# Kernel optimization log

Hardware: AMD Instinct MI355X
Metric: run time of the kernel (lower is better)

## Reference

```python
import jax, jax.numpy as jnp
import numpy as np

D = 128  # embed dim

def linear(x, W, b):
    return x @ W.T + b

def mha1(x, w_in, b_in, w_out, b_out):
    # Single-head MultiheadAttention, x: (S, B, D), seq-first like torch.nn.MultiheadAttention
    q, k, v = jnp.split(x @ w_in.T + b_in, 3, axis=-1)
    scores = jnp.einsum('sbd,tbd->bst', q, k) / jnp.sqrt(jnp.asarray(D, x.dtype))
    att = jax.nn.softmax(scores, axis=-1)
    o = jnp.einsum('bst,tbd->sbd', att, v)
    return o @ w_out.T + b_out

def setup_inputs() -> dict:
    key = jax.random.key(0)
    ks = iter(jax.random.split(key, 32))
    def p(shape, scale=0.02):
        return (jax.random.normal(next(ks), shape, dtype=jnp.float32) * scale)
    B, S, F = 8, 2048, 3584
    inp = {
        'x': jax.random.normal(next(ks), (B, S, F), dtype=jnp.float32),
        'place_W': p((128, 2048)), 'place_b': p((128,)),
        'cast_W': p((128, 512)), 'cast_b': p((128,)),
        'action_W': p((128, 512)), 'action_b': p((128,)),
        'audio_W': p((128, 512)), 'audio_b': p((128,)),
        'e_W': p((128, 512)), 'e_b': p((128,)),
        'la_win': p((3 * D, D)), 'la_bin': p((3 * D,)),
        'la_wout': p((D, D)), 'la_bout': p((D,)),
        'be_W': p((128, 256)), 'be_b': p((128,)),
        'ba_win': p((3 * D, D)), 'ba_bin': p((3 * D,)),
        'ba_wout': p((D, D)), 'ba_bout': p((D,)),
        'bp_W': p((1, 128)), 'bp_b': p((1,)),
    }
    return inp

def reference(x, place_W, place_b, cast_W, cast_b, action_W, action_b,
              audio_W, audio_b, e_W, e_b, la_win, la_bin, la_wout, la_bout,
              be_W, be_b, ba_win, ba_bin, ba_wout, ba_bout, bp_W, bp_b):
    # --- forward_embeddings ---
    place = jax.nn.relu(linear(x[:, :, :2048], place_W, place_b))
    cast = jax.nn.relu(linear(x[:, :, 2048:2560], cast_W, cast_b))
    action = jax.nn.relu(linear(x[:, :, 2560:3072], action_W, action_b))
    audio = jax.nn.relu(linear(x[:, :, 3072:3584], audio_W, audio_b))
    feats = jnp.concatenate((place, cast, action, audio), axis=2)  # (B,S,512)
    e = jax.nn.relu(linear(feats, e_W, e_b))  # (B,S,128)
    e = jnp.transpose(e, (1, 0, 2))  # (S,B,128) seq-first
    e = mha1(e, la_win, la_bin, la_wout, la_bout)
    # --- forward_segmentation (single-pass prefix/suffix means) ---
    S = e.shape[0]
    csum = jnp.cumsum(e, axis=0)  # (S,B,D)
    total = csum[-1]
    i = jnp.arange(1, S, dtype=e.dtype)[:, None, None]
    left = csum[:-1] / i                       # mean of e[:i]
    right = (total[None] - csum[:-1]) / (S - i)  # mean of e[i:]
    cat = jnp.concatenate((left, right), axis=-1)  # (S-1,B,256)
    b = jax.nn.relu(linear(cat, be_W, be_b))
    b = mha1(b, ba_win, ba_bin, ba_wout, ba_bout)
    b = jax.nn.sigmoid(linear(b, bp_W, bp_b))[..., 0]  # (S-1,B)
    return (e, b)
```

## Files before the change

kernel.cpp:

```cpp
#include <hip/hip_runtime.h>
#include <hip/hip_bf16.h>
#include <math.h>
#include <stdint.h>


#define DEV static __device__ __forceinline__

typedef __attribute__((ext_vector_type(8))) short bf16x8;
typedef __attribute__((ext_vector_type(4))) float f32x4;

DEV uint32_t pk2bf(float a, float b) {
  __hip_bfloat162 h = __float22bfloat162_rn(make_float2(a, b));
  return *(uint32_t*)&h;
}
DEV uint2 cvt4(float4 f) {
  return make_uint2(pk2bf(f.x, f.y), pk2bf(f.z, f.w));
}
DEV uint16_t bf1(float a) { return (uint16_t)(pk2bf(a, 0.f) & 0xffffu); }
DEV float frombf(uint16_t h) {
  union { uint32_t u; float f; } v; v.u = ((uint32_t)h) << 16; return v.f;
}

#define OFF_PW      0u
#define OFF_CW      262144u
#define OFF_AW      327680u
#define OFF_UW      393216u
#define OFF_EW      458752u
#define OFF_LAWIN   524288u
#define OFF_LAWOUT  573440u
#define OFF_BEW     589824u
#define OFF_BAWIN   622592u
#define OFF_BAWOUT  671744u
#define OFF_END     688128u

struct WPtrs { const float* p[10]; };

__global__ __launch_bounds__(256) void pack_weights(WPtrs wp, uint16_t* __restrict__ WB)
{
  const uint32_t off[11] = {OFF_PW, OFF_CW, OFF_AW, OFF_UW, OFF_EW, OFF_LAWIN,
                            OFF_LAWOUT, OFF_BEW, OFF_BAWIN, OFF_BAWOUT, OFF_END};
  uint32_t h = (blockIdx.x * 256u + threadIdx.x) * 4u;
  if (h >= OFF_END) return;
  int s = 0;
  while (h >= off[s + 1]) ++s;
  float4 f = *(const float4*)(wp.p[s] + (h - off[s]));
  *(uint2*)(WB + h) = cvt4(f);
}

template<bool ABF, bool OBF, bool RELU, bool REMAP>
__global__ __launch_bounds__(256) void gemm64(
    const void* __restrict__ Ap, int lda,
    const uint16_t* __restrict__ Wb,
    const float* __restrict__ bias,
    void* __restrict__ Cp, int ldc,
    int M, int K)
{
  __shared__ __align__(16) uint16_t As[64 * 72];
  __shared__ __align__(16) uint16_t Ws[128 * 72];

  const int t  = threadIdx.x;
  const int m0 = blockIdx.x * 64;
  const int n0 = blockIdx.y * 128;
  const int w  = t >> 6, l = t & 63;
  const int ln = l & 15, qd = l >> 4;

  f32x4 acc[4][2];
#pragma unroll
  for (int i = 0; i < 4; ++i) { acc[i][0] = (f32x4){0,0,0,0}; acc[i][1] = (f32x4){0,0,0,0}; }

  const int rr = t >> 4;
  const int cl = (t & 15) * 4;
  const int r8 = t >> 3;
  const int c8 = (t & 7) * 8;

  for (int k0 = 0; k0 < K; k0 += 64) {
    __syncthreads();
    if (ABF) {
      const uint16_t* A = (const uint16_t*)Ap;
#pragma unroll
      for (int i = 0; i < 2; ++i) {
        int m = m0 + r8 + 32 * i;
        int mc = m < M ? m : M - 1;
        *(bf16x8*)(As + (size_t)(r8 + 32 * i) * 72 + c8) =
            *(const bf16x8*)(A + (size_t)mc * lda + k0 + c8);
      }
    } else {
      const float* A = (const float*)Ap;
#pragma unroll
      for (int i = 0; i < 4; ++i) {
        int m = m0 + rr + 16 * i;
        int mc = m < M ? m : M - 1;
        float4 f = *(const float4*)(A + (size_t)mc * lda + k0 + cl);
        *(uint2*)(As + (size_t)(rr + 16 * i) * 72 + cl) = cvt4(f);
      }
    }
#pragma unroll
    for (int i = 0; i < 4; ++i) {
      int n = r8 + 32 * i;
      *(bf16x8*)(Ws + (size_t)n * 72 + c8) =
          *(const bf16x8*)(Wb + (size_t)(n0 + n) * K + k0 + c8);
    }
    __syncthreads();
#pragma unroll
    for (int ks = 0; ks < 2; ++ks) {
      bf16x8 af[4], bfr[2];
#pragma unroll
      for (int mf = 0; mf < 4; ++mf)
        af[mf] = *(const bf16x8*)(As + (size_t)(mf * 16 + ln) * 72 + ks * 32 + qd * 8);
#pragma unroll
      for (int nf = 0; nf < 2; ++nf)
        bfr[nf] = *(const bf16x8*)(Ws + (size_t)(w * 32 + nf * 16 + ln) * 72 + ks * 32 + qd * 8);
#pragma unroll
      for (int mf = 0; mf < 4; ++mf)
#pragma unroll
        for (int nf = 0; nf < 2; ++nf)
          acc[mf][nf] = __builtin_amdgcn_mfma_f32_16x16x32_bf16(af[mf], bfr[nf], acc[mf][nf], 0, 0, 0);
    }
  }

#pragma unroll
  for (int mf = 0; mf < 4; ++mf) {
#pragma unroll
    for (int r = 0; r < 4; ++r) {
      int m = m0 + mf * 16 + qd * 4 + r;
      if (m < M) {
        size_t ro = REMAP ? (size_t)((m & 2047) * 8 + (m >> 11)) : (size_t)m;
#pragma unroll
        for (int nf = 0; nf < 2; ++nf) {
          int n = n0 + w * 32 + nf * 16 + ln;
          float v = acc[mf][nf][r] + bias[n];
          if (RELU) v = fmaxf(v, 0.f);
          if (OBF) ((uint16_t*)Cp)[ro * (size_t)ldc + n] = bf1(v);
          else     ((float*)Cp)[ro * (size_t)ldc + n] = v;
        }
      }
    }
  }
}

__global__ __launch_bounds__(256) void gemm_feats64(
    const float* __restrict__ x, const uint16_t* __restrict__ WB,
    const float* __restrict__ pb, const float* __restrict__ cb,
    const float* __restrict__ ab, const float* __restrict__ ub,
    uint16_t* __restrict__ feats)
{
  __shared__ __align__(16) uint16_t As[64 * 72];
  __shared__ __align__(16) uint16_t Ws[128 * 72];

  const int seg = blockIdx.y;
  const uint16_t* Wb; const float* bias; int kbase, Kseg;
  if (seg == 0)      { Wb = WB + OFF_PW; bias = pb; kbase = 0;    Kseg = 2048; }
  else if (seg == 1) { Wb = WB + OFF_CW; bias = cb; kbase = 2048; Kseg = 512; }
  else if (seg == 2) { Wb = WB + OFF_AW; bias = ab; kbase = 2560; Kseg = 512; }
  else               { Wb = WB + OFF_UW; bias = ub; kbase = 3072; Kseg = 512; }

  const int t  = threadIdx.x;
  const int m0 = blockIdx.x * 64;
  const int w  = t >> 6, l = t & 63;
  const int ln = l & 15, qd = l >> 4;

  f32x4 acc[4][2];
#pragma unroll
  for (int i = 0; i < 4; ++i) { acc[i][0] = (f32x4){0,0,0,0}; acc[i][1] = (f32x4){0,0,0,0}; }

  const int rr = t >> 4;
  const int cl = (t & 15) * 4;
  const int r8 = t >> 3;
  const int c8 = (t & 7) * 8;

  for (int k0 = 0; k0 < Kseg; k0 += 64) {
    __syncthreads();
#pragma unroll
    for (int i = 0; i < 4; ++i) {
      int m = m0 + rr + 16 * i;
      float4 f = *(const float4*)(x + (size_t)m * 3584 + kbase + k0 + cl);
      *(uint2*)(As + (size_t)(rr + 16 * i) * 72 + cl) = cvt4(f);
    }
#pragma unroll
    for (int i = 0; i < 4; ++i) {
      int n = r8 + 32 * i;
      *(bf16x8*)(Ws + (size_t)n * 72 + c8) =
          *(const bf16x8*)(Wb + (size_t)n * Kseg + k0 + c8);
    }
    __syncthreads();
#pragma unroll
    for (int ks = 0; ks < 2; ++ks) {
      bf16x8 af[4], bfr[2];
#pragma unroll
      for (int mf = 0; mf < 4; ++mf)
        af[mf] = *(const bf16x8*)(As + (size_t)(mf * 16 + ln) * 72 + ks * 32 + qd * 8);
#pragma unroll
      for (int nf = 0; nf < 2; ++nf)
        bfr[nf] = *(const bf16x8*)(Ws + (size_t)(w * 32 + nf * 16 + ln) * 72 + ks * 32 + qd * 8);
#pragma unroll
      for (int mf = 0; mf < 4; ++mf)
#pragma unroll
        for (int nf = 0; nf < 2; ++nf)
          acc[mf][nf] = __builtin_amdgcn_mfma_f32_16x16x32_bf16(af[mf], bfr[nf], acc[mf][nf], 0, 0, 0);
    }
  }

#pragma unroll
  for (int mf = 0; mf < 4; ++mf) {
#pragma unroll
    for (int r = 0; r < 4; ++r) {
      int m = m0 + mf * 16 + qd * 4 + r;
#pragma unroll
      for (int nf = 0; nf < 2; ++nf) {
        int n = w * 32 + nf * 16 + ln;
        float v = fmaxf(acc[mf][nf][r] + bias[n], 0.f);
        feats[(size_t)m * 512 + seg * 128 + n] = bf1(v);
      }
    }
  }
}

__global__ __launch_bounds__(256) void gemm_becat64(
    const float* __restrict__ csum,
    const uint16_t* __restrict__ Wb, const float* __restrict__ bias,
    uint16_t* __restrict__ C)
{
  __shared__ __align__(16) uint16_t As[64 * 72];
  __shared__ __align__(16) uint16_t Ws[128 * 72];

  const int M = 16376, K = 256;
  const int t  = threadIdx.x;
  const int m0 = blockIdx.x * 64;
  const int w  = t >> 6, l = t & 63;
  const int ln = l & 15, qd = l >> 4;

  f32x4 acc[4][2];
#pragma unroll
  for (int i = 0; i < 4; ++i) { acc[i][0] = (f32x4){0,0,0,0}; acc[i][1] = (f32x4){0,0,0,0}; }

  const int rr = t >> 4;
  const int cl = (t & 15) * 4;
  const int r8 = t >> 3;
  const int c8 = (t & 7) * 8;

  for (int k0 = 0; k0 < K; k0 += 64) {
    __syncthreads();
#pragma unroll
    for (int i = 0; i < 4; ++i) {
      int m = m0 + rr + 16 * i;
      int mc = m < M ? m : M - 1;
      int j = mc >> 3, bb = mc & 7;
      int kk = k0 + cl;
      float4 f;
      if (kk < 128) {
        float4 v = *(const float4*)(csum + (size_t)mc * 128 + kk);
        float s = 1.f / (float)(j + 1);
        f = make_float4(v.x * s, v.y * s, v.z * s, v.w * s);
      } else {
        int d = kk - 128;
        float4 c0 = *(const float4*)(csum + (size_t)mc * 128 + d);
        float4 ct = *(const float4*)(csum + (size_t)(16376 + bb) * 128 + d);
        float s = 1.f / (float)(2047 - j);
        f = make_float4((ct.x - c0.x) * s, (ct.y - c0.y) * s,
                        (ct.z - c0.z) * s, (ct.w - c0.w) * s);
      }
      *(uint2*)(As + (size_t)(rr + 16 * i) * 72 + cl) = cvt4(f);
    }
#pragma unroll
    for (int i = 0; i < 4; ++i) {
      int n = r8 + 32 * i;
      *(bf16x8*)(Ws + (size_t)n * 72 + c8) =
          *(const bf16x8*)(Wb + (size_t)n * K + k0 + c8);
    }
    __syncthreads();
#pragma unroll
    for (int ks = 0; ks < 2; ++ks) {
      bf16x8 af[4], bfr[2];
#pragma unroll
      for (int mf = 0; mf < 4; ++mf)
        af[mf] = *(const bf16x8*)(As + (size_t)(mf * 16 + ln) * 72 + ks * 32 + qd * 8);
#pragma unroll
      for (int nf = 0; nf < 2; ++nf)
        bfr[nf] = *(const bf16x8*)(Ws + (size_t)(w * 32 + nf * 16 + ln) * 72 + ks * 32 + qd * 8);
#pragma unroll
      for (int mf = 0; mf < 4; ++mf)
#pragma unroll
        for (int nf = 0; nf < 2; ++nf)
          acc[mf][nf] = __builtin_amdgcn_mfma_f32_16x16x32_bf16(af[mf], bfr[nf], acc[mf][nf], 0, 0, 0);
    }
  }

#pragma unroll
  for (int mf = 0; mf < 4; ++mf) {
#pragma unroll
    for (int r = 0; r < 4; ++r) {
      int m = m0 + mf * 16 + qd * 4 + r;
      if (m < M) {
#pragma unroll
        for (int nf = 0; nf < 2; ++nf) {
          int n = w * 32 + nf * 16 + ln;
          C[(size_t)m * 128 + n] = bf1(fmaxf(acc[mf][nf][r] + bias[n], 0.f));
        }
      }
    }
  }
}

__global__ __launch_bounds__(256) void vpack(
    const uint16_t* __restrict__ proj, uint16_t* __restrict__ Vtb, int Slen)
{
  __shared__ __align__(16) uint16_t Vs[64][136];

  const int kt = blockIdx.x, b = blockIdx.y, t = threadIdx.x;
  const int sl = t >> 2, cg = (t & 3) * 32;
  const int s  = kt * 64 + sl;
  const int valid = s < Slen;
  const int sc = valid ? s : Slen - 1;
  const uint16_t* src = proj + ((size_t)sc * 8 + b) * 384 + 256 + cg;
#pragma unroll
  for (int i = 0; i < 4; ++i) {
    bf16x8 v;
    if (valid) v = *(const bf16x8*)(src + i * 8);
    else       v = (bf16x8){0,0,0,0,0,0,0,0};
    *(bf16x8*)(&Vs[sl][cg + i * 8]) = v;
  }
  __syncthreads();
  const int d = t >> 1, hh = t & 1;
  uint32_t wv[16];
#pragma unroll
  for (int j = 0; j < 8; ++j) {
    int k0o = hh * 8 + j;
    wv[j * 2]     = (uint32_t)Vs[k0o][d]      | ((uint32_t)Vs[k0o + 16][d] << 16);
    wv[j * 2 + 1] = (uint32_t)Vs[k0o + 32][d] | ((uint32_t)Vs[k0o + 48][d] << 16);
  }
  uint16_t* dv = Vtb + (((size_t)b * 32 + kt) * 128 + d) * 64 + hh * 32;
#pragma unroll
  for (int i = 0; i < 4; ++i)
    *(uint4*)(dv + i * 8) = *(uint4*)(&wv[i * 4]);
}

__global__ __launch_bounds__(256, 3) void attn_split3(
    const uint16_t* __restrict__ proj, const uint16_t* __restrict__ Vtb,
    float* __restrict__ Opart, float* __restrict__ ml, int Slen)
{
  __shared__ __align__(16) uint16_t KsL[64 * 136];
  __shared__ __align__(16) uint16_t VtL[128 * 72];
  __shared__ __align__(16) uint16_t PbL[4][16 * 72];

  const int t  = threadIdx.x;
  const int b  = blockIdx.y;
  const int q0 = blockIdx.x * 64;
  const int split = blockIdx.z;
  const int kbeg = split * 704;
  const int kend = (split == 2) ? Slen : kbeg + 704;
  const int w  = t >> 6;
  const int l  = t & 63;
  const int ln = l & 15;
  const int qd = l >> 4;
  const float scl = 0.08838834764831845f;

  bf16x8 qf[4];
  {
    int qrow = q0 + w * 16 + ln;
    int qc = qrow < Slen ? qrow : Slen - 1;
    const uint16_t* qp = proj + ((size_t)qc * 8 + b) * 384 + qd * 8;
#pragma unroll
    for (int ks = 0; ks < 4; ++ks) {
      union { bf16x8 v; uint16_t h[8]; uint32_t u[4]; } in, out;
      in.v = *(const bf16x8*)(qp + ks * 32);
#pragma unroll
      for (int j = 0; j < 4; ++j)
        out.u[j] = pk2bf(frombf(in.h[2 * j]) * scl, frombf(in.h[2 * j + 1]) * scl);
      qf[ks] = out.v;
    }
  }

  f32x4 oacc[8];
#pragma unroll
  for (int i = 0; i < 8; ++i) oacc[i] = (f32x4){0.f, 0.f, 0.f, 0.f};
  float mrow[4] = {-INFINITY, -INFINITY, -INFINITY, -INFINITY};
  float lrow[4] = {0.f, 0.f, 0.f, 0.f};

  const int ntiles = (kend - kbeg + 63) >> 6;
  for (int kt = 0; kt < ntiles; ++kt) {
    __syncthreads();
    {
      const int key = t >> 2, cg = (t & 3) * 32;
      int kg = kbeg + kt * 64 + key;
      int kc = kg < Slen ? kg : Slen - 1;
      const uint16_t* src = proj + ((size_t)kc * 8 + b) * 384 + 128 + cg;
      uint16_t* dst = KsL + key * 136 + cg;
#pragma unroll
      for (int i = 0; i < 4; ++i)
        *(bf16x8*)(dst + i * 8) = *(const bf16x8*)(src + i * 8);
    }
    {
      const int d = t >> 1, h2 = (t & 1) * 32;
      const int tile = 11 * split + kt;
      const uint16_t* src = Vtb + (((size_t)b * 32 + tile) * 128 + d) * 64 + h2;
      uint16_t* dst = VtL + d * 72 + h2;
#pragma unroll
      for (int i = 0; i < 4; ++i)
        *(bf16x8*)(dst + i * 8) = *(const bf16x8*)(src + i * 8);
    }
    __syncthreads();

    f32x4 sc[4];
#pragma unroll
    for (int nf = 0; nf < 4; ++nf) {
      f32x4 acc = (f32x4){0.f, 0.f, 0.f, 0.f};
#pragma unroll
      for (int ks = 0; ks < 4; ++ks) {
        bf16x8 kf = *(const bf16x8*)(KsL + (size_t)(nf * 16 + ln) * 136 + ks * 32 + qd * 8);
        acc = __builtin_amdgcn_mfma_f32_16x16x32_bf16(qf[ks], kf, acc, 0, 0, 0);
      }
      int key = kbeg + kt * 64 + nf * 16 + ln;
      if (key >= kend) { acc[0] = -1e30f; acc[1] = -1e30f; acc[2] = -1e30f; acc[3] = -1e30f; }
      sc[nf] = acc;
    }

    float alphaR[4];
#pragma unroll
    for (int r = 0; r < 4; ++r) {
      float mx = fmaxf(fmaxf(sc[0][r], sc[1][r]), fmaxf(sc[2][r], sc[3][r]));
      mx = fmaxf(mx, __shfl_xor(mx, 1));
      mx = fmaxf(mx, __shfl_xor(mx, 2));
      mx = fmaxf(mx, __shfl_xor(mx, 4));
      mx = fmaxf(mx, __shfl_xor(mx, 8));
      float mNew = fmaxf(mrow[r], mx);
      float p0 = __expf(sc[0][r] - mNew);
      float p1 = __expf(sc[1][r] - mNew);
      float p2 = __expf(sc[2][r] - mNew);
      float p3 = __expf(sc[3][r] - mNew);
      float ps = p0 + p1 + p2 + p3;
      ps += __shfl_xor(ps, 1);
      ps += __shfl_xor(ps, 2);
      ps += __shfl_xor(ps, 4);
      ps += __shfl_xor(ps, 8);
      float alpha = __expf(mrow[r] - mNew);
      mrow[r] = mNew;
      lrow[r] = lrow[r] * alpha + ps;
      alphaR[r] = alpha;
      uint2 pk;
      pk.x = pk2bf(p0, p1);
      pk.y = pk2bf(p2, p3);
      *(uint2*)(PbL[w] + (size_t)(qd * 4 + r) * 72 + ln * 4) = pk;
    }
#pragma unroll
    for (int no = 0; no < 8; ++no) {
#pragma unroll
      for (int r = 0; r < 4; ++r) oacc[no][r] *= alphaR[r];
    }
    __asm__ volatile("s_waitcnt lgkmcnt(0)" ::: "memory");

#pragma unroll
    for (int ks2 = 0; ks2 < 2; ++ks2) {
      bf16x8 af = *(const bf16x8*)(PbL[w] + (size_t)ln * 72 + ks2 * 32 + qd * 8);
#pragma unroll
      for (int no = 0; no < 8; ++no) {
        bf16x8 vf = *(const bf16x8*)(VtL + (size_t)(no * 16 + ln) * 72 + ks2 * 32 + qd * 8);
        oacc[no] = __builtin_amdgcn_mfma_f32_16x16x32_bf16(af, vf, oacc[no], 0, 0, 0);
      }
    }
  }

#pragma unroll
  for (int r = 0; r < 4; ++r) {
    int qg = q0 + w * 16 + qd * 4 + r;
    if (qg < Slen) {
      size_t row = (size_t)qg * 8 + b;
      float* dst = Opart + ((size_t)split * 16384 + row) * 128 + ln;
#pragma unroll
      for (int no = 0; no < 8; ++no) dst[no * 16] = oacc[no][r];
      if (ln == 0) {
        ml[((size_t)split * 16384 + row) * 2 + 0] = mrow[r];
        ml[((size_t)split * 16384 + row) * 2 + 1] = lrow[r];
      }
    }
  }
}

__global__ __launch_bounds__(256) void attn_combine3(
    const float* __restrict__ Opart, const float* __restrict__ ml,
    uint16_t* __restrict__ out, int rows)
{
  int idx = blockIdx.x * 256 + threadIdx.x;
  int row = idx >> 5;
  int d   = (idx & 31) * 4;
  if (row >= rows) return;
  float m0 = ml[(size_t)row * 2],                 l0 = ml[(size_t)row * 2 + 1];
  float m1 = ml[((size_t)16384 + row) * 2],       l1 = ml[((size_t)16384 + row) * 2 + 1];
  float m2 = ml[((size_t)32768 + row) * 2],       l2 = ml[((size_t)32768 + row) * 2 + 1];
  float M = fmaxf(fmaxf(m0, m1), m2);
  float w0 = __expf(m0 - M), w1 = __expf(m1 - M), w2 = __expf(m2 - M);
  float inv = 1.f / (l0 * w0 + l1 * w1 + l2 * w2);
  float4 a = *(const float4*)(Opart + (size_t)row * 128 + d);
  float4 c = *(const float4*)(Opart + ((size_t)16384 + row) * 128 + d);
  float4 e = *(const float4*)(Opart + ((size_t)32768 + row) * 128 + d);
  float4 o = make_float4((a.x * w0 + c.x * w1 + e.x * w2) * inv,
                         (a.y * w0 + c.y * w1 + e.y * w2) * inv,
                         (a.z * w0 + c.z * w1 + e.z * w2) * inv,
                         (a.w * w0 + c.w * w1 + e.w * w2) * inv);
  *(uint2*)(out + (size_t)row * 128 + d) = cvt4(o);
}

__global__ void cumsum_p1(const float* __restrict__ e, float* __restrict__ csum,
                          float* __restrict__ part)
{
  int chunk = blockIdx.x, b = blockIdx.y, d = threadIdx.x;
  float run = 0.f;
  int s0 = chunk * 64;
  for (int s = 0; s < 64; ++s) {
    size_t idx = ((size_t)(s0 + s) * 8 + b) * 128 + d;
    run += e[idx];
    csum[idx] = run;
  }
  part[(b * 32 + chunk) * 128 + d] = run;
}

__global__ void cumsum_p2(float* __restrict__ part)
{
  int b = blockIdx.x, d = threadIdx.x;
  float run = 0.f;
  for (int c = 0; c < 32; ++c) {
    float v = part[(b * 32 + c) * 128 + d];
    part[(b * 32 + c) * 128 + d] = run;
    run += v;
  }
}

__global__ void cumsum_p3(float* __restrict__ csum, const float* __restrict__ part)
{
  int chunk = blockIdx.x, b = blockIdx.y, d = threadIdx.x;
  float off = part[(b * 32 + chunk) * 128 + d];
  int s0 = chunk * 64;
  for (int s = 0; s < 64; ++s)
    csum[((size_t)(s0 + s) * 8 + b) * 128 + d] += off;
}

__global__ __launch_bounds__(256) void gemm_bout_head(
    const uint16_t* __restrict__ A,
    const uint16_t* __restrict__ Wb,
    const float* __restrict__ bias,
    const float* __restrict__ bpW, const float* __restrict__ bpb,
    float* __restrict__ out, int M)
{
  __shared__ __align__(16) uint16_t As[64 * 72];
  __shared__ __align__(16) uint16_t Ws[128 * 72];
  __shared__ float Ct[64][133];

  const int K = 128;
  const int t  = threadIdx.x;
  const int m0 = blockIdx.x * 64;
  const int w  = t >> 6, l = t & 63;
  const int ln = l & 15, qd = l >> 4;

  f32x4 acc[4][2];
#pragma unroll
  for (int i = 0; i < 4; ++i) { acc[i][0] = (f32x4){0,0,0,0}; acc[i][1] = (f32x4){0,0,0,0}; }

  const int r8 = t >> 3;
  const int c8 = (t & 7) * 8;

  for (int k0 = 0; k0 < K; k0 += 64) {
    __syncthreads();
#pragma unroll
    for (int i = 0; i < 2; ++i) {
      int m = m0 + r8 + 32 * i;
      int mc = m < M ? m : M - 1;
      *(bf16x8*)(As + (size_t)(r8 + 32 * i) * 72 + c8) =
          *(const bf16x8*)(A + (size_t)mc * 128 + k0 + c8);
    }
#pragma unroll
    for (int i = 0; i < 4; ++i) {
      int n = r8 + 32 * i;
      *(bf16x8*)(Ws + (size_t)n * 72 + c8) =
          *(const bf16x8*)(Wb + (size_t)n * K + k0 + c8);
    }
    __syncthreads();
#pragma unroll
    for (int ks = 0; ks < 2; ++ks) {
      bf16x8 af[4], bfr[2];
#pragma unroll
      for (int mf = 0; mf < 4; ++mf)
        af[mf] = *(const bf16x8*)(As + (size_t)(mf * 16 + ln) * 72 + ks * 32 + qd * 8);
#pragma unroll
      for (int nf = 0; nf < 2; ++nf)
        bfr[nf] = *(const bf16x8*)(Ws + (size_t)(w * 32 + nf * 16 + ln) * 72 + ks * 32 + qd * 8);
#pragma unroll
      for (int mf = 0; mf < 4; ++mf)
#pragma unroll
        for (int nf = 0; nf < 2; ++nf)
          acc[mf][nf] = __builtin_amdgcn_mfma_f32_16x16x32_bf16(af[mf], bfr[nf], acc[mf][nf], 0, 0, 0);
    }
  }

  __syncthreads();
#pragma unroll
  for (int mf = 0; mf < 4; ++mf) {
#pragma unroll
    for (int r = 0; r < 4; ++r) {
      int rowL = mf * 16 + qd * 4 + r;
#pragma unroll
      for (int nf = 0; nf < 2; ++nf) {
        int n = w * 32 + nf * 16 + ln;
        Ct[rowL][n] = acc[mf][nf][r] + bias[n];
      }
    }
  }
  __syncthreads();
  {
    int row = t >> 2, qg = t & 3;
    int m = m0 + row;
    float p = 0.f;
#pragma unroll
    for (int j = 0; j < 32; ++j) {
      int c = qg + j * 4;
      p += Ct[row][c] * bpW[c];
    }
    p += __shfl_xor(p, 1);
    p += __shfl_xor(p, 2);
    if (qg == 0 && m < M)
      out[m] = 1.f / (1.f + __expf(-(p + bpb[0])));
  }
}

extern "C" void kernel_launch(void* const* d_in, const int* in_sizes, int n_in,
                              void* d_out, int out_size, void* d_ws, size_t ws_size,
                              hipStream_t stream)
{
  const float* x       = (const float*)d_in[0];
  const float* pW      = (const float*)d_in[1];
  const float* pb      = (const float*)d_in[2];
  const float* cW      = (const float*)d_in[3];
  const float* cb      = (const float*)d_in[4];
  const float* aW      = (const float*)d_in[5];
  const float* ab      = (const float*)d_in[6];
  const float* uW      = (const float*)d_in[7];
  const float* ub      = (const float*)d_in[8];
  const float* eW      = (const float*)d_in[9];
  const float* eb      = (const float*)d_in[10];
  const float* la_win  = (const float*)d_in[11];
  const float* la_bin  = (const float*)d_in[12];
  const float* la_wout = (const float*)d_in[13];
  const float* la_bout = (const float*)d_in[14];
  const float* beW     = (const float*)d_in[15];
  const float* beb     = (const float*)d_in[16];
  const float* ba_win  = (const float*)d_in[17];
  const float* ba_bin  = (const float*)d_in[18];
  const float* ba_wout = (const float*)d_in[19];
  const float* ba_bout = (const float*)d_in[20];
  const float* bpW     = (const float*)d_in[21];
  const float* bpb     = (const float*)d_in[22];

  float* ws   = (float*)d_ws;
  float* outF = (float*)d_out;

  uint16_t* WB  = (uint16_t*)ws;
  float* base   = ws + 344064;
  uint16_t* featsB = (uint16_t*)base;
  float* csumB  = base;
  float* partB  = base + 2097152;
  uint16_t* eB  = (uint16_t*)(base + 4194304);
  uint16_t* projB = (uint16_t*)(base + 5242880);
  uint16_t* VtbB  = (uint16_t*)(base + 8388608);
  float* OpartB = base + 9437184;
  float* mlB    = base + 15728640;

  WPtrs wp;
  wp.p[0] = pW; wp.p[1] = cW; wp.p[2] = aW; wp.p[3] = uW; wp.p[4] = eW;
  wp.p[5] = la_win; wp.p[6] = la_wout; wp.p[7] = beW; wp.p[8] = ba_win; wp.p[9] = ba_wout;
  pack_weights<<<dim3(672), 256, 0, stream>>>(wp, WB);

  gemm_feats64<<<dim3(256, 4), 256, 0, stream>>>(x, WB, pb, cb, ab, ub, featsB);
  gemm64<true, true, true, true><<<dim3(256, 1), 256, 0, stream>>>(
      featsB, 512, WB + OFF_EW, eb, eB, 128, 16384, 512);
  gemm64<true, true, false, false><<<dim3(256, 3), 256, 0, stream>>>(
      eB, 128, WB + OFF_LAWIN, la_bin, projB, 384, 16384, 128);
  vpack<<<dim3(32, 8), 256, 0, stream>>>(projB, VtbB, 2048);
  attn_split3<<<dim3(32, 8, 3), 256, 0, stream>>>(projB, VtbB, OpartB, mlB, 2048);
  attn_combine3<<<dim3(2048), 256, 0, stream>>>(OpartB, mlB, eB, 16384);
  gemm64<true, false, false, false><<<dim3(256, 1), 256, 0, stream>>>(
      eB, 128, WB + OFF_LAWOUT, la_bout, outF, 128, 16384, 128);
  cumsum_p1<<<dim3(32, 8), 128, 0, stream>>>(outF, csumB, partB);
  cumsum_p2<<<dim3(8), 128, 0, stream>>>(partB);
  cumsum_p3<<<dim3(32, 8), 128, 0, stream>>>(csumB, partB);
  gemm_becat64<<<dim3(256), 256, 0, stream>>>(csumB, WB + OFF_BEW, beb, eB);
  gemm64<true, true, false, false><<<dim3(256, 3), 256, 0, stream>>>(
      eB, 128, WB + OFF_BAWIN, ba_bin, projB, 384, 16376, 128);
  vpack<<<dim3(32, 8), 256, 0, stream>>>(projB, VtbB, 2047);
  attn_split3<<<dim3(32, 8, 3), 256, 0, stream>>>(projB, VtbB, OpartB, mlB, 2047);
  attn_combine3<<<dim3(2047), 256, 0, stream>>>(OpartB, mlB, eB, 16376);
  gemm_bout_head<<<dim3(256), 256, 0, stream>>>(
      eB, WB + OFF_BAWOUT, ba_bout, bpW, bpb, outF + 2097152, 16376);
}
```

Measured before the change: 553.4 us.

## Fuse attention combine into out-proj GEMM, fold cumsum fixup, prefetch K/V

The split-attention combine step now happens inside the output-projection GEMM's A-tile load, which drops the separate combine kernel and its bf16 round trip for both attention blocks. The third cumsum pass is removed: the boundary GEMM adds the per-chunk prefix offsets itself, and the cumsum now uses 32-row chunks to launch more blocks. The attention kernel also register-prefetches the next K/V tile while the current one is computed. In exchange the GEMM does extra reads of three Opart slices and the partial array, and the prefetch raises register pressure.

Result: faster. 537.2 us (-2.9%).

```diff
diff --git a/kernel.cpp b/kernel.cpp
--- a/kernel.cpp
+++ b/kernel.cpp
@@ -216,7 +216,7 @@
 }
 
 __global__ __launch_bounds__(256) void gemm_becat64(
-    const float* __restrict__ csum,
+    const float* __restrict__ csum, const float* __restrict__ part,
     const uint16_t* __restrict__ Wb, const float* __restrict__ bias,
     uint16_t* __restrict__ C)
 {
@@ -249,15 +249,21 @@
       float4 f;
       if (kk < 128) {
         float4 v = *(const float4*)(csum + (size_t)mc * 128 + kk);
+        float4 p = *(const float4*)(part + (size_t)(bb * 64 + (j >> 5)) * 128 + kk);
         float s = 1.f / (float)(j + 1);
-        f = make_float4(v.x * s, v.y * s, v.z * s, v.w * s);
+        f = make_float4((v.x + p.x) * s, (v.y + p.y) * s,
+                        (v.z + p.z) * s, (v.w + p.w) * s);
       } else {
         int d = kk - 128;
         float4 c0 = *(const float4*)(csum + (size_t)mc * 128 + d);
+        float4 p0 = *(const float4*)(part + (size_t)(bb * 64 + (j >> 5)) * 128 + d);
         float4 ct = *(const float4*)(csum + (size_t)(16376 + bb) * 128 + d);
+        float4 pt = *(const float4*)(part + (size_t)(bb * 64 + 63) * 128 + d);
         float s = 1.f / (float)(2047 - j);
-        f = make_float4((ct.x - c0.x) * s, (ct.y - c0.y) * s,
-                        (ct.z - c0.z) * s, (ct.w - c0.w) * s);
+        f = make_float4(((ct.x + pt.x) - (c0.x + p0.x)) * s,
+                        ((ct.y + pt.y) - (c0.y + p0.y)) * s,
+                        ((ct.z + pt.z) - (c0.z + p0.z)) * s,
+                        ((ct.w + pt.w) - (c0.w + p0.w)) * s);
       }
       *(uint2*)(As + (size_t)(rr + 16 * i) * 72 + cl) = cvt4(f);
     }
@@ -354,6 +360,9 @@
   const int qd = l >> 4;
   const float scl = 0.08838834764831845f;
 
+  const int kkey = t >> 2, kcg = (t & 3) * 32;
+  const int vd   = t >> 1, vh  = (t & 1) * 32;
+
   bf16x8 qf[4];
   {
     int qrow = q0 + w * 16 + ln;
@@ -377,26 +386,39 @@
   float lrow[4] = {0.f, 0.f, 0.f, 0.f};
 
   const int ntiles = (kend - kbeg + 63) >> 6;
+
+  bf16x8 kreg[4], vreg[4];
+  {
+    int kg = kbeg + kkey;
+    int kc = kg < Slen ? kg : Slen - 1;
+    const uint16_t* ksrc = proj + ((size_t)kc * 8 + b) * 384 + 128 + kcg;
+#pragma unroll
+    for (int i = 0; i < 4; ++i) kreg[i] = *(const bf16x8*)(ksrc + i * 8);
+    const uint16_t* vsrc = Vtb + (((size_t)b * 32 + 11 * split) * 128 + vd) * 64 + vh;
+#pragma unroll
+    for (int i = 0; i < 4; ++i) vreg[i] = *(const bf16x8*)(vsrc + i * 8);
+  }
+
   for (int kt = 0; kt < ntiles; ++kt) {
     __syncthreads();
     {
-      const int key = t >> 2, cg = (t & 3) * 32;
-      int kg = kbeg + kt * 64 + key;
+      uint16_t* kdst = KsL + kkey * 136 + kcg;
+#pragma unroll
+      for (int i = 0; i < 4; ++i) *(bf16x8*)(kdst + i * 8) = kreg[i];
+      uint16_t* vdst = VtL + vd * 72 + vh;
+#pragma unroll
+      for (int i = 0; i < 4; ++i) *(bf16x8*)(vdst + i * 8) = vreg[i];
+    }
+    if (kt + 1 < ntiles) {
+      int kg = kbeg + (kt + 1) * 64 + kkey;
       int kc = kg < Slen ? kg : Slen - 1;
-      const uint16_t* src = proj + ((size_t)kc * 8 + b) * 384 + 128 + cg;
-      uint16_t* dst = KsL + key * 136 + cg;
-#pragma unroll
-      for (int i = 0; i < 4; ++i)
-        *(bf16x8*)(dst + i * 8) = *(const bf16x8*)(src + i * 8);
-    }
-    {
-      const int d = t >> 1, h2 = (t & 1) * 32;
-      const int tile = 11 * split + kt;
-      const uint16_t* src = Vtb + (((size_t)b * 32 + tile) * 128 + d) * 64 + h2;
-      uint16_t* dst = VtL + d * 72 + h2;
-#pragma unroll
-      for (int i = 0; i < 4; ++i)
-        *(bf16x8*)(dst + i * 8) = *(const bf16x8*)(src + i * 8);
+      const uint16_t* ksrc = proj + ((size_t)kc * 8 + b) * 384 + 128 + kcg;
+#pragma unroll
+      for (int i = 0; i < 4; ++i) kreg[i] = *(const bf16x8*)(ksrc + i * 8);
+      const int tile = 11 * split + kt + 1;
+      const uint16_t* vsrc = Vtb + (((size_t)b * 32 + tile) * 128 + vd) * 64 + vh;
+#pragma unroll
+      for (int i = 0; i < 4; ++i) vreg[i] = *(const bf16x8*)(vsrc + i * 8);
     }
     __syncthreads();
 
@@ -475,66 +497,9 @@
   }
 }
 
-__global__ __launch_bounds__(256) void attn_combine3(
+template<bool HEAD>
+__global__ __launch_bounds__(256) void gemm_attc64(
     const float* __restrict__ Opart, const float* __restrict__ ml,
-    uint16_t* __restrict__ out, int rows)
-{
-  int idx = blockIdx.x * 256 + threadIdx.x;
-  int row = idx >> 5;
-  int d   = (idx & 31) * 4;
-  if (row >= rows) return;
-  float m0 = ml[(size_t)row * 2],                 l0 = ml[(size_t)row * 2 + 1];
-  float m1 = ml[((size_t)16384 + row) * 2],       l1 = ml[((size_t)16384 + row) * 2 + 1];
-  float m2 = ml[((size_t)32768 + row) * 2],       l2 = ml[((size_t)32768 + row) * 2 + 1];
-  float M = fmaxf(fmaxf(m0, m1), m2);
-  float w0 = __expf(m0 - M), w1 = __expf(m1 - M), w2 = __expf(m2 - M);
-  float inv = 1.f / (l0 * w0 + l1 * w1 + l2 * w2);
-  float4 a = *(const float4*)(Opart + (size_t)row * 128 + d);
-  float4 c = *(const float4*)(Opart + ((size_t)16384 + row) * 128 + d);
-  float4 e = *(const float4*)(Opart + ((size_t)32768 + row) * 128 + d);
-  float4 o = make_float4((a.x * w0 + c.x * w1 + e.x * w2) * inv,
-                         (a.y * w0 + c.y * w1 + e.y * w2) * inv,
-                         (a.z * w0 + c.z * w1 + e.z * w2) * inv,
-                         (a.w * w0 + c.w * w1 + e.w * w2) * inv);
-  *(uint2*)(out + (size_t)row * 128 + d) = cvt4(o);
-}
-
-__global__ void cumsum_p1(const float* __restrict__ e, float* __restrict__ csum,
-                          float* __restrict__ part)
-{
-  int chunk = blockIdx.x, b = blockIdx.y, d = threadIdx.x;
-  float run = 0.f;
-  int s0 = chunk * 64;
-  for (int s = 0; s < 64; ++s) {
-    size_t idx = ((size_t)(s0 + s) * 8 + b) * 128 + d;
-    run += e[idx];
-    csum[idx] = run;
-  }
-  part[(b * 32 + chunk) * 128 + d] = run;
-}
-
-__global__ void cumsum_p2(float* __restrict__ part)
-{
-  int b = blockIdx.x, d = threadIdx.x;
-  float run = 0.f;
-  for (int c = 0; c < 32; ++c) {
-    float v = part[(b * 32 + c) * 128 + d];
-    part[(b * 32 + c) * 128 + d] = run;
-    run += v;
-  }
-}
-
-__global__ void cumsum_p3(float* __restrict__ csum, const float* __restrict__ part)
-{
-  int chunk = blockIdx.x, b = blockIdx.y, d = threadIdx.x;
-  float off = part[(b * 32 + chunk) * 128 + d];
-  int s0 = chunk * 64;
-  for (int s = 0; s < 64; ++s)
-    csum[((size_t)(s0 + s) * 8 + b) * 128 + d] += off;
-}
-
-__global__ __launch_bounds__(256) void gemm_bout_head(
-    const uint16_t* __restrict__ A,
     const uint16_t* __restrict__ Wb,
     const float* __restrict__ bias,
     const float* __restrict__ bpW, const float* __restrict__ bpb,
@@ -542,7 +507,8 @@
 {
   __shared__ __align__(16) uint16_t As[64 * 72];
   __shared__ __align__(16) uint16_t Ws[128 * 72];
-  __shared__ float Ct[64][133];
+  __shared__ float RW[64][4];
+  __shared__ float Ct[HEAD ? 64 : 1][133];
 
   const int K = 128;
   const int t  = threadIdx.x;
@@ -550,21 +516,44 @@
   const int w  = t >> 6, l = t & 63;
   const int ln = l & 15, qd = l >> 4;
 
+  if (t < 64) {
+    int m = m0 + t;
+    int mc = m < M ? m : M - 1;
+    float m0v = ml[(size_t)mc * 2],                 l0 = ml[(size_t)mc * 2 + 1];
+    float m1v = ml[((size_t)16384 + mc) * 2],       l1 = ml[((size_t)16384 + mc) * 2 + 1];
+    float m2v = ml[((size_t)32768 + mc) * 2],       l2 = ml[((size_t)32768 + mc) * 2 + 1];
+    float Mx = fmaxf(fmaxf(m0v, m1v), m2v);
+    float w0 = __expf(m0v - Mx), w1 = __expf(m1v - Mx), w2 = __expf(m2v - Mx);
+    RW[t][0] = w0; RW[t][1] = w1; RW[t][2] = w2;
+    RW[t][3] = 1.f / (l0 * w0 + l1 * w1 + l2 * w2);
+  }
+
   f32x4 acc[4][2];
 #pragma unroll
   for (int i = 0; i < 4; ++i) { acc[i][0] = (f32x4){0,0,0,0}; acc[i][1] = (f32x4){0,0,0,0}; }
 
+  const int rr = t >> 4;
+  const int cl = (t & 15) * 4;
   const int r8 = t >> 3;
   const int c8 = (t & 7) * 8;
 
   for (int k0 = 0; k0 < K; k0 += 64) {
     __syncthreads();
 #pragma unroll
-    for (int i = 0; i < 2; ++i) {
-      int m = m0 + r8 + 32 * i;
+    for (int i = 0; i < 4; ++i) {
+      int m = m0 + rr + 16 * i;
       int mc = m < M ? m : M - 1;
-      *(bf16x8*)(As + (size_t)(r8 + 32 * i) * 72 + c8) =
-          *(const bf16x8*)(A + (size_t)mc * 128 + k0 + c8);
+      int kk = k0 + cl;
+      float4 a = *(const float4*)(Opart + (size_t)mc * 128 + kk);
+      float4 c = *(const float4*)(Opart + ((size_t)16384 + mc) * 128 + kk);
+      float4 e = *(const float4*)(Opart + ((size_t)32768 + mc) * 128 + kk);
+      int rl = rr + 16 * i;
+      float w0 = RW[rl][0], w1 = RW[rl][1], w2 = RW[rl][2], inv = RW[rl][3];
+      float4 f = make_float4((a.x * w0 + c.x * w1 + e.x * w2) * inv,
+                             (a.y * w0 + c.y * w1 + e.y * w2) * inv,
+                             (a.z * w0 + c.z * w1 + e.z * w2) * inv,
+                             (a.w * w0 + c.w * w1 + e.w * w2) * inv);
+      *(uint2*)(As + (size_t)rl * 72 + cl) = cvt4(f);
     }
 #pragma unroll
     for (int i = 0; i < 4; ++i) {
@@ -590,21 +579,21 @@
     }
   }
 
-  __syncthreads();
-#pragma unroll
-  for (int mf = 0; mf < 4; ++mf) {
-#pragma unroll
-    for (int r = 0; r < 4; ++r) {
-      int rowL = mf * 16 + qd * 4 + r;
-#pragma unroll
-      for (int nf = 0; nf < 2; ++nf) {
-        int n = w * 32 + nf * 16 + ln;
-        Ct[rowL][n] = acc[mf][nf][r] + bias[n];
-      }
-    }
-  }
-  __syncthreads();
-  {
+  if (HEAD) {
+    __syncthreads();
+#pragma unroll
+    for (int mf = 0; mf < 4; ++mf) {
+#pragma unroll
+      for (int r = 0; r < 4; ++r) {
+        int rowL = mf * 16 + qd * 4 + r;
+#pragma unroll
+        for (int nf = 0; nf < 2; ++nf) {
+          int n = w * 32 + nf * 16 + ln;
+          Ct[rowL][n] = acc[mf][nf][r] + bias[n];
+        }
+      }
+    }
+    __syncthreads();
     int row = t >> 2, qg = t & 3;
     int m = m0 + row;
     float p = 0.f;
@@ -617,6 +606,46 @@
     p += __shfl_xor(p, 2);
     if (qg == 0 && m < M)
       out[m] = 1.f / (1.f + __expf(-(p + bpb[0])));
+  } else {
+#pragma unroll
+    for (int mf = 0; mf < 4; ++mf) {
+#pragma unroll
+      for (int r = 0; r < 4; ++r) {
+        int m = m0 + mf * 16 + qd * 4 + r;
+        if (m < M) {
+#pragma unroll
+          for (int nf = 0; nf < 2; ++nf) {
+            int n = w * 32 + nf * 16 + ln;
+            out[(size_t)m * 128 + n] = acc[mf][nf][r] + bias[n];
+          }
+        }
+      }
+    }
+  }
+}
+
+__global__ void cumsum_p1(const float* __restrict__ e, float* __restrict__ csum,
+                          float* __restrict__ part)
+{
+  int chunk = blockIdx.x, b = blockIdx.y, d = threadIdx.x;
+  float run = 0.f;
+  int s0 = chunk * 32;
+  for (int s = 0; s < 32; ++s) {
+    size_t idx = ((size_t)(s0 + s) * 8 + b) * 128 + d;
+    run += e[idx];
+    csum[idx] = run;
+  }
+  part[(b * 64 + chunk) * 128 + d] = run;
+}
+
+__global__ void cumsum_p2(float* __restrict__ part)
+{
+  int b = blockIdx.x, d = threadIdx.x;
+  float run = 0.f;
+  for (int c = 0; c < 64; ++c) {
+    float v = part[(b * 64 + c) * 128 + d];
+    part[(b * 64 + c) * 128 + d] = run;
+    run += v;
   }
 }
 
@@ -674,18 +703,15 @@
       eB, 128, WB + OFF_LAWIN, la_bin, projB, 384, 16384, 128);
   vpack<<<dim3(32, 8), 256, 0, stream>>>(projB, VtbB, 2048);
   attn_split3<<<dim3(32, 8, 3), 256, 0, stream>>>(projB, VtbB, OpartB, mlB, 2048);
-  attn_combine3<<<dim3(2048), 256, 0, stream>>>(OpartB, mlB, eB, 16384);
-  gemm64<true, false, false, false><<<dim3(256, 1), 256, 0, stream>>>(
-      eB, 128, WB + OFF_LAWOUT, la_bout, outF, 128, 16384, 128);
-  cumsum_p1<<<dim3(32, 8), 128, 0, stream>>>(outF, csumB, partB);
+  gemm_attc64<false><<<dim3(256), 256, 0, stream>>>(
+      OpartB, mlB, WB + OFF_LAWOUT, la_bout, nullptr, nullptr, outF, 16384);
+  cumsum_p1<<<dim3(64, 8), 128, 0, stream>>>(outF, csumB, partB);
   cumsum_p2<<<dim3(8), 128, 0, stream>>>(partB);
-  cumsum_p3<<<dim3(32, 8), 128, 0, stream>>>(csumB, partB);
-  gemm_becat64<<<dim3(256), 256, 0, stream>>>(csumB, WB + OFF_BEW, beb, eB);
+  gemm_becat64<<<dim3(256), 256, 0, stream>>>(csumB, partB, WB + OFF_BEW, beb, eB);
   gemm64<true, true, false, false><<<dim3(256, 3), 256, 0, stream>>>(
       eB, 128, WB + OFF_BAWIN, ba_bin, projB, 384, 16376, 128);
   vpack<<<dim3(32, 8), 256, 0, stream>>>(projB, VtbB, 2047);
   attn_split3<<<dim3(32, 8, 3), 256, 0, stream>>>(projB, VtbB, OpartB, mlB, 2047);
-  attn_combine3<<<dim3(2047), 256, 0, stream>>>(OpartB, mlB, eB, 16376);
-  gemm_bout_head<<<dim3(256), 256, 0, stream>>>(
-      eB, WB + OFF_BAWOUT, ba_bout, bpW, bpb, outF + 2097152, 16376);
-}
+  gemm_attc64<true><<<dim3(256), 256, 0, stream>>>(
+      OpartB, mlB, WB + OFF_BAWOUT, ba_bout, bpW, bpb, outF + 2097152, 16376);
+}
```
